# Kernel optimization log

Hardware: AMD Instinct MI355X
Metric: run time of the kernel (lower is better)

Reference implementation:

```python
import jax, jax.numpy as jnp
import numpy as np

B, F, D, H = 2048, 32, 64, 64

def setup_inputs() -> dict:
    key = jax.random.key(0)
    k1, k2, k3 = jax.random.split(key, 3)
    x = jax.random.normal(k1, (B, F, D), dtype=jnp.float32)
    W1 = jax.random.normal(k2, (D, H), dtype=jnp.float32) * 0.01
    b1 = jnp.zeros((H,), dtype=jnp.float32)
    Ws = jax.random.normal(k3, (H, 1), dtype=jnp.float32) * 0.01
    bs = jnp.zeros((1,), dtype=jnp.float32)
    return {"x": x, "W1": W1, "b1": b1, "Ws": Ws, "bs": bs}

def reference(x, W1, b1, Ws, bs):
    # pairwise field interactions: cross[b, p, d] = x[b, i_p, d] * x[b, j_p, d]
    f = x.shape[1]
    ii, jj = np.triu_indices(f, k=1)  # P = f*(f-1)/2 pairs
    cross = x[:, ii, :] * x[:, jj, :]            # [B, P, D]
    # small MLP (DNN with one hidden layer, relu, dropout disabled in eval)
    h = jax.nn.relu(jnp.einsum('bpd,dh->bph', cross, W1) + b1)  # [B, P, H]
    # attention score per pair, softmax over pairs
    scores = (jnp.einsum('bph,ho->bpo', h, Ws) + bs).squeeze(-1)  # [B, P]
    attn = jax.nn.softmax(scores, axis=-1)                        # [B, P]
    pool = jnp.sum(cross * attn[:, :, None], axis=1)              # [B, D]
    afm = jnp.sum(pool, axis=1, keepdims=True)                    # [B, 1]
    return afm
```

## Files before the change

### kernel.cpp

```cpp
#include <hip/hip_runtime.h>


#define F 32
#define D 64
#define H 64
#define P 496
#define NT 4
#define MT 31
#define XPAD 68

typedef __attribute__((ext_vector_type(8))) short bf16x8;
typedef __attribute__((ext_vector_type(4))) float f32x4;

__device__ inline short f2bf(float f) {
    union { float f; unsigned u; } v; v.f = f;
    unsigned r = v.u + 0x7FFFu + ((v.u >> 16) & 1u);
    return (short)(r >> 16);
}

__global__ __launch_bounds__(256) void afm_kernel(
    const float* __restrict__ x, const float* __restrict__ W1,
    const float* __restrict__ b1, const float* __restrict__ Ws,
    const float* __restrict__ bs, float* __restrict__ out)
{
    __shared__ float xs[F][XPAD];
    __shared__ short iis[512], jjs[512];
    __shared__ float scores[512];
    __shared__ float svals[512];
    __shared__ float b1s[H], wss[H];
    __shared__ float redmax[4], rednum[4], redden[4];

    const int tid  = threadIdx.x;
    const int b    = blockIdx.x;
    const int lane = tid & 63;
    const int wid  = tid >> 6;
    const int l15  = lane & 15;
    const int quad = lane >> 4;

    const float* xb = x + (size_t)b * (F * D);
    for (int idx = tid; idx < F * D; idx += 256)
        xs[idx >> 6][idx & 63] = xb[idx];
    if (tid < H) { b1s[tid] = b1[tid]; wss[tid] = Ws[tid]; }
    for (int p = tid; p < P; p += 256) {
        int i = 0, rem = p;
        while (rem >= F - 1 - i) { rem -= F - 1 - i; ++i; }
        iis[p] = (short)i; jjs[p] = (short)(i + 1 + rem);
    }
    const float bsv = bs[0];
    __syncthreads();

    bf16x8 bfrag[NT][2];
    #pragma unroll
    for (int nt = 0; nt < NT; ++nt)
        #pragma unroll
        for (int ks = 0; ks < 2; ++ks)
            #pragma unroll
            for (int j8 = 0; j8 < 8; ++j8) {
                int k = quad * 8 + j8 + ks * 32;
                int n = nt * 16 + l15;
                bfrag[nt][ks][j8] = f2bf(W1[k * H + n]);
            }

    for (int t = wid; t < MT; t += 4) {
        const int p0 = t * 16;
        const int p  = p0 + l15;
        const int ip = iis[p], jp = jjs[p];

        bf16x8 afrag[2];
        float ssum = 0.f;
        #pragma unroll
        for (int ks = 0; ks < 2; ++ks) {
            const int kb = quad * 8 + ks * 32;
            float4 xi0 = *(const float4*)&xs[ip][kb];
            float4 xi1 = *(const float4*)&xs[ip][kb + 4];
            float4 xj0 = *(const float4*)&xs[jp][kb];
            float4 xj1 = *(const float4*)&xs[jp][kb + 4];
            float c[8];
            c[0] = xi0.x * xj0.x; c[1] = xi0.y * xj0.y;
            c[2] = xi0.z * xj0.z; c[3] = xi0.w * xj0.w;
            c[4] = xi1.x * xj1.x; c[5] = xi1.y * xj1.y;
            c[6] = xi1.z * xj1.z; c[7] = xi1.w * xj1.w;
            #pragma unroll
            for (int j8 = 0; j8 < 8; ++j8) {
                ssum += c[j8];
                afrag[ks][j8] = f2bf(c[j8]);
            }
        }
        ssum += __shfl_xor(ssum, 16, 64);
        ssum += __shfl_xor(ssum, 32, 64);
        if (quad == 0) svals[p] = ssum;

        f32x4 acc[NT];
        #pragma unroll
        for (int nt = 0; nt < NT; ++nt) { f32x4 z = {0.f,0.f,0.f,0.f}; acc[nt] = z; }
        #pragma unroll
        for (int ks = 0; ks < 2; ++ks)
            #pragma unroll
            for (int nt = 0; nt < NT; ++nt)
                acc[nt] = __builtin_amdgcn_mfma_f32_16x16x32_bf16(
                              afrag[ks], bfrag[nt][ks], acc[nt], 0, 0, 0);

        float sp[4] = {0.f, 0.f, 0.f, 0.f};
        #pragma unroll
        for (int nt = 0; nt < NT; ++nt) {
            const int n = nt * 16 + l15;
            const float bb = b1s[n], ww = wss[n];
            #pragma unroll
            for (int reg = 0; reg < 4; ++reg) {
                float v = acc[nt][reg] + bb;
                v = v > 0.f ? v : 0.f;
                sp[reg] += v * ww;
            }
        }
        #pragma unroll
        for (int reg = 0; reg < 4; ++reg) {
            float s = sp[reg];
            s += __shfl_xor(s, 1, 64);
            s += __shfl_xor(s, 2, 64);
            s += __shfl_xor(s, 4, 64);
            s += __shfl_xor(s, 8, 64);
            if (l15 == 0) scores[p0 + quad * 4 + reg] = s + bsv;
        }
    }
    __syncthreads();

    float m = -1e30f;
    for (int p = tid; p < P; p += 256) m = fmaxf(m, scores[p]);
    #pragma unroll
    for (int off = 32; off >= 1; off >>= 1) m = fmaxf(m, __shfl_xor(m, off, 64));
    if (lane == 0) redmax[wid] = m;
    __syncthreads();
    m = fmaxf(fmaxf(redmax[0], redmax[1]), fmaxf(redmax[2], redmax[3]));

    float num = 0.f, den = 0.f;
    for (int p = tid; p < P; p += 256) {
        float e = __expf(scores[p] - m);
        num += e * svals[p];
        den += e;
    }
    #pragma unroll
    for (int off = 32; off >= 1; off >>= 1) {
        num += __shfl_xor(num, off, 64);
        den += __shfl_xor(den, off, 64);
    }
    if (lane == 0) { rednum[wid] = num; redden[wid] = den; }
    __syncthreads();
    if (tid == 0) {
        float nn = rednum[0] + rednum[1] + rednum[2] + rednum[3];
        float dd = redden[0] + redden[1] + redden[2] + redden[3];
        out[b] = nn / dd;
    }
}

extern "C" void kernel_launch(void* const* d_in, const int* in_sizes, int n_in,
                              void* d_out, int out_size, void* d_ws, size_t ws_size,
                              hipStream_t stream) {
    const float* x  = (const float*)d_in[0];
    const float* W1 = (const float*)d_in[1];
    const float* b1 = (const float*)d_in[2];
    const float* Ws = (const float*)d_in[3];
    const float* bs = (const float*)d_in[4];
    float* out = (float*)d_out;
    const int B = in_sizes[0] / (F * D);
    afm_kernel<<<B, 256, 0, stream>>>(x, W1, b1, Ws, bs, out);
}
```

Measured before the change: 100.2 us.

## Store x as bf16 in LDS, compute pair sums via MFMA, DPP reductions

```diff
diff --git a/kernel.cpp b/kernel.cpp
--- a/kernel.cpp
+++ b/kernel.cpp
@@ -7,27 +7,39 @@
 #define P 496
 #define NT 4
 #define MT 31
-#define XPAD 68
+#define RB 72
 
 typedef __attribute__((ext_vector_type(8))) short bf16x8;
 typedef __attribute__((ext_vector_type(4))) float f32x4;
 
-__device__ inline short f2bf(float f) {
-    union { float f; unsigned u; } v; v.f = f;
-    unsigned r = v.u + 0x7FFFu + ((v.u >> 16) & 1u);
-    return (short)(r >> 16);
+__device__ inline unsigned rne_hi(float f) {
+    unsigned u = __float_as_uint(f);
+    return u + 0x7FFFu + ((u >> 16) & 1u);
+}
+__device__ inline int pack_rne(float a, float b) {
+    return (int)__builtin_amdgcn_perm(rne_hi(b), rne_hi(a), 0x07060302u);
+}
+__device__ inline int prodpk(int ri, int rj) {
+    float a0 = __int_as_float(ri << 16);
+    float a1 = __int_as_float(ri & 0xFFFF0000);
+    float b0 = __int_as_float(rj << 16);
+    float b1 = __int_as_float(rj & 0xFFFF0000);
+    return pack_rne(a0 * b0, a1 * b1);
 }
 
-__global__ __launch_bounds__(256) void afm_kernel(
+#define DPP_ADD(v, ctrl) ((v) + __int_as_float(__builtin_amdgcn_update_dpp( \
+        0, __float_as_int(v), (ctrl), 0xF, 0xF, true)))
+
+__global__ __launch_bounds__(256, 4) void afm_kernel(
     const float* __restrict__ x, const float* __restrict__ W1,
     const float* __restrict__ b1, const float* __restrict__ Ws,
     const float* __restrict__ bs, float* __restrict__ out)
 {
-    __shared__ float xs[F][XPAD];
-    __shared__ short iis[512], jjs[512];
+    __shared__ short xs[F * RB];
+    __shared__ int   pairtab[512];
     __shared__ float scores[512];
     __shared__ float svals[512];
-    __shared__ float b1s[H], wss[H];
+    __shared__ float2 bw[H];
     __shared__ float redmax[4], rednum[4], redden[4];
 
     const int tid  = threadIdx.x;
@@ -37,14 +49,19 @@
     const int l15  = lane & 15;
     const int quad = lane >> 4;
 
-    const float* xb = x + (size_t)b * (F * D);
-    for (int idx = tid; idx < F * D; idx += 256)
-        xs[idx >> 6][idx & 63] = xb[idx];
-    if (tid < H) { b1s[tid] = b1[tid]; wss[tid] = Ws[tid]; }
+    const float4* xb4 = (const float4*)(x + (size_t)b * (F * D));
+    for (int v = tid; v < (F * D) / 4; v += 256) {
+        float4 w = xb4[v];
+        int row = v >> 4, col = (v & 15) * 4;
+        int lo = pack_rne(w.x, w.y), hi = pack_rne(w.z, w.w);
+        *(int2*)&xs[row * RB + col] = make_int2(lo, hi);
+    }
+    if (tid < H) bw[tid] = make_float2(b1[tid], Ws[tid]);
     for (int p = tid; p < P; p += 256) {
         int i = 0, rem = p;
         while (rem >= F - 1 - i) { rem -= F - 1 - i; ++i; }
-        iis[p] = (short)i; jjs[p] = (short)(i + 1 + rem);
+        int j = i + 1 + rem;
+        pairtab[p] = (i * RB * 2) << 16 | (j * RB * 2);
     }
     const float bsv = bs[0];
     __syncthreads();
@@ -57,69 +74,74 @@
             #pragma unroll
             for (int j8 = 0; j8 < 8; ++j8) {
                 int k = quad * 8 + j8 + ks * 32;
-                int n = nt * 16 + l15;
-                bfrag[nt][ks][j8] = f2bf(W1[k * H + n]);
+                unsigned u = rne_hi(W1[k * H + nt * 16 + l15]);
+                bfrag[nt][ks][j8] = (short)(u >> 16);
             }
+    const short onev = (l15 == 0) ? (short)0x3F80 : (short)0;
+    const bf16x8 onesf = {onev, onev, onev, onev, onev, onev, onev, onev};
+
+    float bb[NT], ww[NT];
+    #pragma unroll
+    for (int nt = 0; nt < NT; ++nt) {
+        float2 t = bw[nt * 16 + l15];
+        bb[nt] = t.x; ww[nt] = t.y;
+    }
+
+    const char* xsb = (const char*)xs;
 
     for (int t = wid; t < MT; t += 4) {
         const int p0 = t * 16;
-        const int p  = p0 + l15;
-        const int ip = iis[p], jp = jjs[p];
+        const int pk = pairtab[p0 + l15];
+        const int io = ((unsigned)pk) >> 16;
+        const int jo = pk & 0xFFFF;
+        const int qb = quad << 4;
 
-        bf16x8 afrag[2];
-        float ssum = 0.f;
-        #pragma unroll
-        for (int ks = 0; ks < 2; ++ks) {
-            const int kb = quad * 8 + ks * 32;
-            float4 xi0 = *(const float4*)&xs[ip][kb];
-            float4 xi1 = *(const float4*)&xs[ip][kb + 4];
-            float4 xj0 = *(const float4*)&xs[jp][kb];
-            float4 xj1 = *(const float4*)&xs[jp][kb + 4];
-            float c[8];
-            c[0] = xi0.x * xj0.x; c[1] = xi0.y * xj0.y;
-            c[2] = xi0.z * xj0.z; c[3] = xi0.w * xj0.w;
-            c[4] = xi1.x * xj1.x; c[5] = xi1.y * xj1.y;
-            c[6] = xi1.z * xj1.z; c[7] = xi1.w * xj1.w;
-            #pragma unroll
-            for (int j8 = 0; j8 < 8; ++j8) {
-                ssum += c[j8];
-                afrag[ks][j8] = f2bf(c[j8]);
-            }
-        }
-        ssum += __shfl_xor(ssum, 16, 64);
-        ssum += __shfl_xor(ssum, 32, 64);
-        if (quad == 0) svals[p] = ssum;
+        int4 xi0 = *(const int4*)(xsb + io + qb);
+        int4 xj0 = *(const int4*)(xsb + jo + qb);
+        int4 xi1 = *(const int4*)(xsb + io + 64 + qb);
+        int4 xj1 = *(const int4*)(xsb + jo + 64 + qb);
+
+        union { int i[4]; bf16x8 v; } A0, A1;
+        A0.i[0] = prodpk(xi0.x, xj0.x); A0.i[1] = prodpk(xi0.y, xj0.y);
+        A0.i[2] = prodpk(xi0.z, xj0.z); A0.i[3] = prodpk(xi0.w, xj0.w);
+        A1.i[0] = prodpk(xi1.x, xj1.x); A1.i[1] = prodpk(xi1.y, xj1.y);
+        A1.i[2] = prodpk(xi1.z, xj1.z); A1.i[3] = prodpk(xi1.w, xj1.w);
 
         f32x4 acc[NT];
         #pragma unroll
         for (int nt = 0; nt < NT; ++nt) { f32x4 z = {0.f,0.f,0.f,0.f}; acc[nt] = z; }
+        f32x4 accs = {0.f, 0.f, 0.f, 0.f};
+
         #pragma unroll
-        for (int ks = 0; ks < 2; ++ks)
-            #pragma unroll
-            for (int nt = 0; nt < NT; ++nt)
-                acc[nt] = __builtin_amdgcn_mfma_f32_16x16x32_bf16(
-                              afrag[ks], bfrag[nt][ks], acc[nt], 0, 0, 0);
+        for (int nt = 0; nt < NT; ++nt)
+            acc[nt] = __builtin_amdgcn_mfma_f32_16x16x32_bf16(A0.v, bfrag[nt][0], acc[nt], 0, 0, 0);
+        accs = __builtin_amdgcn_mfma_f32_16x16x32_bf16(A0.v, onesf, accs, 0, 0, 0);
+        #pragma unroll
+        for (int nt = 0; nt < NT; ++nt)
+            acc[nt] = __builtin_amdgcn_mfma_f32_16x16x32_bf16(A1.v, bfrag[nt][1], acc[nt], 0, 0, 0);
+        accs = __builtin_amdgcn_mfma_f32_16x16x32_bf16(A1.v, onesf, accs, 0, 0, 0);
 
-        float sp[4] = {0.f, 0.f, 0.f, 0.f};
-        #pragma unroll
-        for (int nt = 0; nt < NT; ++nt) {
-            const int n = nt * 16 + l15;
-            const float bb = b1s[n], ww = wss[n];
-            #pragma unroll
-            for (int reg = 0; reg < 4; ++reg) {
-                float v = acc[nt][reg] + bb;
-                v = v > 0.f ? v : 0.f;
-                sp[reg] += v * ww;
-            }
-        }
+        float spr[4];
         #pragma unroll
         for (int reg = 0; reg < 4; ++reg) {
-            float s = sp[reg];
-            s += __shfl_xor(s, 1, 64);
-            s += __shfl_xor(s, 2, 64);
-            s += __shfl_xor(s, 4, 64);
-            s += __shfl_xor(s, 8, 64);
-            if (l15 == 0) scores[p0 + quad * 4 + reg] = s + bsv;
+            float s = 0.f;
+            #pragma unroll
+            for (int nt = 0; nt < NT; ++nt) {
+                float v = acc[nt][reg] + bb[nt];
+                v = v > 0.f ? v : 0.f;
+                s += v * ww[nt];
+            }
+            s = DPP_ADD(s, 0xB1);
+            s = DPP_ADD(s, 0x4E);
+            s = DPP_ADD(s, 0x141);
+            s = DPP_ADD(s, 0x140);
+            spr[reg] = s;
+        }
+        if (l15 == 0) {
+            *(float4*)&svals[p0 + quad * 4] =
+                make_float4(accs[0], accs[1], accs[2], accs[3]);
+            *(float4*)&scores[p0 + quad * 4] =
+                make_float4(spr[0] + bsv, spr[1] + bsv, spr[2] + bsv, spr[3] + bsv);
         }
     }
     __syncthreads();
```

Measured after the change: 94.79 us. -5.4%, faster.
